# Optimization experiments

Hardware: AMD Instinct MI355X
Metric: run time of the kernel (lower is better)

## Reference

```python
import jax, jax.numpy as jnp
import numpy as np

NEG_SLOPE = 0.2


def gat_conv(x, edge_index, W, a_src, a_dst, b):
    # PyG GATConv (heads=1, add_self_loops=True, concat -> out_channels)
    N = x.shape[0]
    h = x @ W                                   # [N, F_out]
    loops = jnp.arange(N, dtype=edge_index.dtype)
    src = jnp.concatenate([edge_index[0], loops])   # message sources (x_j)
    dst = jnp.concatenate([edge_index[1], loops])   # message targets (x_i)
    # attention logits: e = LeakyReLU(a_src . h_j + a_dst . h_i)
    alpha_s = h @ a_src                          # [N]
    alpha_d = h @ a_dst                          # [N]
    e = jax.nn.leaky_relu(alpha_s[src] + alpha_d[dst], NEG_SLOPE)  # [E+N]
    # segment softmax over incoming edges of each dst node
    m = jax.ops.segment_max(e, dst, num_segments=N)
    e = jnp.exp(e - m[dst])
    denom = jax.ops.segment_sum(e, dst, num_segments=N)
    alpha = e / denom[dst]                       # self-loops guarantee denom > 0
    # weighted scatter-sum aggregation
    out = jax.ops.segment_sum(alpha[:, None] * h[src], dst, num_segments=N)
    return out + b


def setup_inputs() -> dict:
    key = jax.random.key(0)
    ks = jax.random.split(key, 10)
    N, E, F_in, H, F_out = 100000, 3200000, 54, 16, 16
    x = jax.random.normal(ks[0], (N, F_in), dtype=jnp.float32)
    edge_index = jax.random.randint(ks[1], (2, E), 0, N, dtype=jnp.int64)
    s1 = 1.0 / np.sqrt(F_in)
    s2 = 1.0 / np.sqrt(H)
    return {
        "x": x,
        "edge_index": edge_index,
        "W1": jax.random.uniform(ks[2], (F_in, H), jnp.float32, -s1, s1),
        "a1_src": jax.random.uniform(ks[3], (H,), jnp.float32, -s2, s2),
        "a1_dst": jax.random.uniform(ks[4], (H,), jnp.float32, -s2, s2),
        "b1": jnp.zeros((H,), jnp.float32),
        "W2": jax.random.uniform(ks[5], (H, F_out), jnp.float32, -s2, s2),
        "a2_src": jax.random.uniform(ks[6], (F_out,), jnp.float32, -0.25, 0.25),
        "a2_dst": jax.random.uniform(ks[7], (F_out,), jnp.float32, -0.25, 0.25),
        "b2": jnp.zeros((F_out,), jnp.float32),
    }


def reference(x, edge_index, W1, a1_src, a1_dst, b1, W2, a2_src, a2_dst, b2):
    h = gat_conv(x, edge_index, W1, a1_src, a1_dst, b1)
    h = jax.nn.elu(h)
    # dropout p=0.5 is identity in eval mode
    out = gat_conv(h, edge_index, W2, a2_src, a2_dst, b2)
    return out
```

## Files before the change

kernel.cpp:

```cpp
#include <hip/hip_runtime.h>
#include <hip/hip_bf16.h>

typedef __hip_bfloat16 bf16;

static constexpr int N_NODES = 100000;
static constexpr int N_EDGES = 3200000;
static constexpr int F_IN    = 54;
static constexpr int F_HID   = 16;

static constexpr int BSHIFT    = 7;
static constexpr int BNODES    = 128;
static constexpr int NBUCK     = (N_NODES + BNODES - 1) / BNODES;
static constexpr int CAP_B     = 5120;
static constexpr int BIN_CHUNK = 8192;
static constexpr int GRDB      = (N_EDGES + BIN_CHUNK - 1) / BIN_CHUNK;
static constexpr int GRDN_F    = (N_NODES + 1023) / 1024;

static constexpr size_t WS_FLAGS  = 0;
static constexpr size_t WS_ASRC   = 4;
static constexpr size_t WS_ADST   = 100004;
static constexpr size_t WS_ASRC2  = 200004;
static constexpr size_t WS_ADST2  = 300004;
static constexpr size_t WS_BCNT   = 400004;
static constexpr size_t WS_ROWBEG = 401028;
static constexpr size_t WS_ROWCNT = 501028;
static constexpr size_t WS_HBUF   = 601028;
static constexpr size_t WS_ZBUF   = 2201028;
static constexpr size_t WS_BEDGES = 3801028;
static constexpr size_t WS_SRCS   = 7804868;
static constexpr size_t WS_BUCKET_END = WS_SRCS + (size_t)NBUCK * CAP_B;
static constexpr size_t WS_ATOMIC_END = WS_ZBUF + 1600000;

__device__ __forceinline__ float lrelu(float v) { return v >= 0.f ? v : 0.2f * v; }
__device__ __forceinline__ float loadf(const void* p, int i, bool f32) {
    return f32 ? ((const float*)p)[i] : __bfloat162float(((const bf16*)p)[i]);
}

__global__ __launch_bounds__(256) void k_probe0(
    const void* __restrict__ x, const void* __restrict__ ei,
    int* __restrict__ flags, int* __restrict__ bcnt)
{
    __shared__ int cnt, nz;
    const int t = threadIdx.x;
    if (t == 0) { cnt = 0; nz = 0; }
    __syncthreads();
    const unsigned u = ((const unsigned*)x)[t];
    if ((u & 0x7FFFu) >= 0x4800u) atomicAdd(&cnt, 1);
    if (t < 64) {
        if (((const unsigned*)ei)[2 * t + 1] != 0u) atomicAdd(&nz, 1);
    }
    for (int i = t; i < 1024; i += 256) bcnt[i] = 0;
    __syncthreads();
    if (t == 0) flags[0] = ((cnt >= 16) ? 1 : 0) | ((nz == 0) ? 2 : 0);
}

__global__ __launch_bounds__(1024, 8) void k_binfeat(
    const void* __restrict__ ei, const void* __restrict__ x,
    const void* __restrict__ W1, const void* __restrict__ a_s,
    const void* __restrict__ a_d, const int* __restrict__ flags,
    int* __restrict__ bcnt, int* __restrict__ bedges,
    float* __restrict__ hbuf, float* __restrict__ asrc, float* __restrict__ adst)
{
    __shared__ int            hist[NBUCK];
    __shared__ int            base[NBUCK];
    __shared__ int            cval[BIN_CHUNK];
    __shared__ unsigned short cbkt[BIN_CHUNK];
    __shared__ float Wl[F_IN * F_HID];
    __shared__ float asl[F_HID];
    __shared__ float adl[F_HID];
    const int t = threadIdx.x;
    const bool f32 = flags[0] & 1;
    const bool i64 = flags[0] & 2;

    if (blockIdx.x < GRDB) {
        const int e0 = blockIdx.x * BIN_CHUNK;
        const int valid = min(BIN_CHUNK, N_EDGES - e0);
        for (int i = t; i < NBUCK; i += 1024) hist[i] = 0;
        __syncthreads();
#pragma unroll
        for (int i = 0; i < BIN_CHUNK / 1024; ++i) {
            const int idx = i * 1024 + t;
            const int e = e0 + idx;
            if (idx < valid) {
                int s, d;
                if (i64) {
                    s = ((const int*)ei)[2 * (size_t)e];
                    d = ((const int*)ei)[2 * ((size_t)N_EDGES + e)];
                } else {
                    s = ((const int*)ei)[e];
                    d = ((const int*)ei)[(size_t)N_EDGES + e];
                }
                const int b = d >> BSHIFT;
                cval[idx] = (s << BSHIFT) | (d & (BNODES - 1));
                cbkt[idx] = (unsigned short)b;
                atomicAdd(&hist[b], 1);
            }
        }
        __syncthreads();
        for (int i = t; i < NBUCK; i += 1024) {
            const int c = hist[i];
            base[i] = c ? atomicAdd(&bcnt[i], c) : 0;
            hist[i] = 0;
        }
        __syncthreads();
#pragma unroll
        for (int i = 0; i < BIN_CHUNK / 1024; ++i) {
            const int idx = i * 1024 + t;
            if (idx < valid) {
                const int b = cbkt[idx];
                const int r = atomicAdd(&hist[b], 1);
                const int pos = base[b] + r;
                if (pos < CAP_B) bedges[(size_t)b * CAP_B + pos] = cval[idx];
            }
        }
    } else {
        for (int i = t; i < F_IN * F_HID; i += 1024) Wl[i] = loadf(W1, i, f32);
        if (t < F_HID) { asl[t] = loadf(a_s, t, f32); adl[t] = loadf(a_d, t, f32); }
        __syncthreads();
        const int node = (blockIdx.x - GRDB) * 1024 + t;
        if (node >= N_NODES) return;

        float h[F_HID];
#pragma unroll
        for (int k = 0; k < F_HID; ++k) h[k] = 0.f;
        if (f32) {
            const float2* xp = (const float2*)((const float*)x + (size_t)node * F_IN);
#pragma unroll
            for (int j = 0; j < F_IN / 2; ++j) {
                const float2 v = xp[j];
#pragma unroll
                for (int k = 0; k < F_HID; ++k) {
                    h[k] = fmaf(v.x, Wl[(2*j)   * F_HID + k], h[k]);
                    h[k] = fmaf(v.y, Wl[(2*j+1) * F_HID + k], h[k]);
                }
            }
        } else {
            const unsigned* xu = (const unsigned*)x + (size_t)node * (F_IN / 2);
#pragma unroll
            for (int j = 0; j < F_IN / 2; ++j) {
                const unsigned u = xu[j];
                const float v0 = __uint_as_float(u << 16);
                const float v1 = __uint_as_float(u & 0xFFFF0000u);
#pragma unroll
                for (int k = 0; k < F_HID; ++k) {
                    h[k] = fmaf(v0, Wl[(2*j)   * F_HID + k], h[k]);
                    h[k] = fmaf(v1, Wl[(2*j+1) * F_HID + k], h[k]);
                }
            }
        }
        float s = 0.f, d = 0.f;
#pragma unroll
        for (int k = 0; k < F_HID; ++k) { s = fmaf(h[k], asl[k], s); d = fmaf(h[k], adl[k], d); }
        asrc[node] = s; adst[node] = d;
        float4* hb = (float4*)(hbuf + (size_t)node * F_HID);
#pragma unroll
        for (int q = 0; q < 4; ++q)
            hb[q] = make_float4(h[4*q], h[4*q+1], h[4*q+2], h[4*q+3]);
    }
}

__global__ __launch_bounds__(512) void k_bsort(
    const int* __restrict__ bcnt, const int* __restrict__ bedges,
    int* __restrict__ rowbeg, int* __restrict__ rowcnt, int* __restrict__ srcs)
{
    __shared__ int hist[BNODES];
    __shared__ int scan[BNODES];
    __shared__ int cur[BNODES];
    const int t = threadIdx.x;
    const int b = blockIdx.x;
    const int n0 = b << BSHIFT;
    if (t < BNODES) hist[t] = 0;
    __syncthreads();
    const int cnt = min(bcnt[b], CAP_B);
    const int* be = bedges + (size_t)b * CAP_B;
    for (int e = t; e < cnt; e += 512)
        atomicAdd(&hist[be[e] & (BNODES - 1)], 1);
    __syncthreads();
    if (t < BNODES) scan[t] = (hist[t] + 3) & ~3;
    __syncthreads();
#pragma unroll
    for (int off = 1; off < BNODES; off <<= 1) {
        const int v = (t < BNODES && t >= off) ? scan[t - off] : 0;
        __syncthreads();
        if (t < BNODES) scan[t] += v;
        __syncthreads();
    }
    if (t < BNODES) {
        const int ex = scan[t] - ((hist[t] + 3) & ~3);
        cur[t] = ex;
        const int node = n0 + t;
        if (node < N_NODES) {
            rowbeg[node] = b * CAP_B + ex;
            rowcnt[node] = hist[t];
        }
    }
    __syncthreads();
    for (int e = t; e < cnt; e += 512) {
        const int p = be[e];
        const int dl = p & (BNODES - 1);
        const int r = atomicAdd(&cur[dl], 1);
        if (r < CAP_B) srcs[(size_t)b * CAP_B + r] = p >> BSHIFT;
    }
}

__global__ __launch_bounds__(256) void k_agg1(
    const int* __restrict__ rowbeg, const int* __restrict__ rowcnt,
    const int* __restrict__ srcs,
    const float* __restrict__ asrc, const float* __restrict__ adst,
    const float* __restrict__ h, const void* __restrict__ b1,
    const void* __restrict__ W2, const void* __restrict__ a_s2,
    const void* __restrict__ a_d2, const int* __restrict__ flags,
    float* __restrict__ h2buf, float* __restrict__ asrc2, float* __restrict__ adst2)
{
    __shared__ float Wl[F_HID * F_HID];
    __shared__ float asl[F_HID];
    __shared__ float adl[F_HID];
    __shared__ float bl[F_HID];
    const bool f32 = flags[0] & 1;
    const int t = threadIdx.x;
    if (t < F_HID * F_HID) Wl[t] = loadf(W2, t, f32);
    if (t < F_HID) {
        asl[t] = loadf(a_s2, t, f32);
        adl[t] = loadf(a_d2, t, f32);
        bl[t]  = loadf(b1, t, f32);
    }
    __syncthreads();

    const int k = t & 15;
    const int node = blockIdx.x * 16 + (t >> 4);
    const float adn = adst[node];
    const float w0 = __expf(lrelu(asrc[node] + adn));
    float denom = w0;
    float acc = w0 * h[(size_t)node * F_HID + k];
    const int n = rowcnt[node];
    const int* sp = srcs + rowbeg[node];
    int i = 0;
    for (; i + 8 <= n; i += 8) {
        const int4 sa = *(const int4*)(sp + i);
        const int4 sb = *(const int4*)(sp + i + 4);
        const float a0 = asrc[sa.x], a1 = asrc[sa.y], a2 = asrc[sa.z], a3 = asrc[sa.w];
        const float a4 = asrc[sb.x], a5 = asrc[sb.y], a6 = asrc[sb.z], a7 = asrc[sb.w];
        const float h0 = h[(size_t)sa.x * F_HID + k];
        const float h1 = h[(size_t)sa.y * F_HID + k];
        const float h2 = h[(size_t)sa.z * F_HID + k];
        const float h3 = h[(size_t)sa.w * F_HID + k];
        const float h4 = h[(size_t)sb.x * F_HID + k];
        const float h5 = h[(size_t)sb.y * F_HID + k];
        const float h6 = h[(size_t)sb.z * F_HID + k];
        const float h7 = h[(size_t)sb.w * F_HID + k];
        const float e0 = __expf(lrelu(a0 + adn));
        const float e1 = __expf(lrelu(a1 + adn));
        const float e2 = __expf(lrelu(a2 + adn));
        const float e3 = __expf(lrelu(a3 + adn));
        const float e4 = __expf(lrelu(a4 + adn));
        const float e5 = __expf(lrelu(a5 + adn));
        const float e6 = __expf(lrelu(a6 + adn));
        const float e7 = __expf(lrelu(a7 + adn));
        denom += (e0 + e1 + e2 + e3) + (e4 + e5 + e6 + e7);
        acc = fmaf(e0, h0, acc); acc = fmaf(e1, h1, acc);
        acc = fmaf(e2, h2, acc); acc = fmaf(e3, h3, acc);
        acc = fmaf(e4, h4, acc); acc = fmaf(e5, h5, acc);
        acc = fmaf(e6, h6, acc); acc = fmaf(e7, h7, acc);
    }
    for (; i + 4 <= n; i += 4) {
        const int4 sa = *(const int4*)(sp + i);
        const float a0 = asrc[sa.x], a1 = asrc[sa.y], a2 = asrc[sa.z], a3 = asrc[sa.w];
        const float h0 = h[(size_t)sa.x * F_HID + k];
        const float h1 = h[(size_t)sa.y * F_HID + k];
        const float h2 = h[(size_t)sa.z * F_HID + k];
        const float h3 = h[(size_t)sa.w * F_HID + k];
        const float e0 = __expf(lrelu(a0 + adn));
        const float e1 = __expf(lrelu(a1 + adn));
        const float e2 = __expf(lrelu(a2 + adn));
        const float e3 = __expf(lrelu(a3 + adn));
        denom += (e0 + e1) + (e2 + e3);
        acc = fmaf(e0, h0, acc); acc = fmaf(e1, h1, acc);
        acc = fmaf(e2, h2, acc); acc = fmaf(e3, h3, acc);
    }
    for (; i < n; ++i) {
        const int s = sp[i];
        const float w = __expf(lrelu(asrc[s] + adn));
        denom += w;
        acc = fmaf(w, h[(size_t)s * F_HID + k], acc);
    }
    float z = acc / denom + bl[k];
    z = z > 0.f ? z : expm1f(z);

    float hh = 0.f;
#pragma unroll
    for (int j = 0; j < F_HID; ++j) {
        const float zj = __shfl(z, j, 16);
        hh = fmaf(zj, Wl[j * F_HID + k], hh);
    }
    float s2 = hh * asl[k], d2 = hh * adl[k];
#pragma unroll
    for (int off = 1; off < 16; off <<= 1) {
        s2 += __shfl_xor(s2, off, 16);
        d2 += __shfl_xor(d2, off, 16);
    }
    h2buf[(size_t)node * F_HID + k] = hh;
    if (k == 0) { asrc2[node] = s2; adst2[node] = d2; }
}

__global__ __launch_bounds__(256) void k_agg2(
    const int* __restrict__ rowbeg, const int* __restrict__ rowcnt,
    const int* __restrict__ srcs,
    const float* __restrict__ asrc, const float* __restrict__ adst,
    const float* __restrict__ h, const void* __restrict__ b2,
    const int* __restrict__ flags, float* __restrict__ outp)
{
    const bool f32 = flags[0] & 1;
    const int t = threadIdx.x;
    const int k = t & 15;
    const int node = blockIdx.x * 16 + (t >> 4);
    const float adn = adst[node];
    const float w0 = __expf(lrelu(asrc[node] + adn));
    float denom = w0;
    float acc = w0 * h[(size_t)node * F_HID + k];
    const int n = rowcnt[node];
    const int* sp = srcs + rowbeg[node];
    int i = 0;
    for (; i + 8 <= n; i += 8) {
        const int4 sa = *(const int4*)(sp + i);
        const int4 sb = *(const int4*)(sp + i + 4);
        const float a0 = asrc[sa.x], a1 = asrc[sa.y], a2 = asrc[sa.z], a3 = asrc[sa.w];
        const float a4 = asrc[sb.x], a5 = asrc[sb.y], a6 = asrc[sb.z], a7 = asrc[sb.w];
        const float h0 = h[(size_t)sa.x * F_HID + k];
        const float h1 = h[(size_t)sa.y * F_HID + k];
        const float h2 = h[(size_t)sa.z * F_HID + k];
        const float h3 = h[(size_t)sa.w * F_HID + k];
        const float h4 = h[(size_t)sb.x * F_HID + k];
        const float h5 = h[(size_t)sb.y * F_HID + k];
        const float h6 = h[(size_t)sb.z * F_HID + k];
        const float h7 = h[(size_t)sb.w * F_HID + k];
        const float e0 = __expf(lrelu(a0 + adn));
        const float e1 = __expf(lrelu(a1 + adn));
        const float e2 = __expf(lrelu(a2 + adn));
        const float e3 = __expf(lrelu(a3 + adn));
        const float e4 = __expf(lrelu(a4 + adn));
        const float e5 = __expf(lrelu(a5 + adn));
        const float e6 = __expf(lrelu(a6 + adn));
        const float e7 = __expf(lrelu(a7 + adn));
        denom += (e0 + e1 + e2 + e3) + (e4 + e5 + e6 + e7);
        acc = fmaf(e0, h0, acc); acc = fmaf(e1, h1, acc);
        acc = fmaf(e2, h2, acc); acc = fmaf(e3, h3, acc);
        acc = fmaf(e4, h4, acc); acc = fmaf(e5, h5, acc);
        acc = fmaf(e6, h6, acc); acc = fmaf(e7, h7, acc);
    }
    for (; i + 4 <= n; i += 4) {
        const int4 sa = *(const int4*)(sp + i);
        const float a0 = asrc[sa.x], a1 = asrc[sa.y], a2 = asrc[sa.z], a3 = asrc[sa.w];
        const float h0 = h[(size_t)sa.x * F_HID + k];
        const float h1 = h[(size_t)sa.y * F_HID + k];
        const float h2 = h[(size_t)sa.z * F_HID + k];
        const float h3 = h[(size_t)sa.w * F_HID + k];
        const float e0 = __expf(lrelu(a0 + adn));
        const float e1 = __expf(lrelu(a1 + adn));
        const float e2 = __expf(lrelu(a2 + adn));
        const float e3 = __expf(lrelu(a3 + adn));
        denom += (e0 + e1) + (e2 + e3);
        acc = fmaf(e0, h0, acc); acc = fmaf(e1, h1, acc);
        acc = fmaf(e2, h2, acc); acc = fmaf(e3, h3, acc);
    }
    for (; i < n; ++i) {
        const int s = sp[i];
        const float w = __expf(lrelu(asrc[s] + adn));
        denom += w;
        acc = fmaf(w, h[(size_t)s * F_HID + k], acc);
    }
    outp[(size_t)node * F_HID + k] = acc / denom + loadf(b2, k, f32);
}

__global__ __launch_bounds__(256) void k_feat1(
    const void* __restrict__ x, const void* __restrict__ W1,
    const void* __restrict__ a_s, const void* __restrict__ a_d,
    const int* __restrict__ flags,
    float* __restrict__ hbuf, float* __restrict__ asrc, float* __restrict__ adst)
{
    const bool f32 = flags[0] & 1;
    __shared__ float Wl[F_IN * F_HID];
    __shared__ float asl[F_HID];
    __shared__ float adl[F_HID];
    const int t = threadIdx.x;
    for (int i = t; i < F_IN * F_HID; i += 256) Wl[i] = loadf(W1, i, f32);
    if (t < F_HID) { asl[t] = loadf(a_s, t, f32); adl[t] = loadf(a_d, t, f32); }
    __syncthreads();
    const int node = blockIdx.x * 256 + t;
    if (node >= N_NODES) return;
    float h[F_HID];
#pragma unroll
    for (int k = 0; k < F_HID; ++k) h[k] = 0.f;
    if (f32) {
        const float2* xp = (const float2*)((const float*)x + (size_t)node * F_IN);
#pragma unroll
        for (int j = 0; j < F_IN / 2; ++j) {
            const float2 v = xp[j];
#pragma unroll
            for (int k = 0; k < F_HID; ++k) {
                h[k] = fmaf(v.x, Wl[(2*j)   * F_HID + k], h[k]);
                h[k] = fmaf(v.y, Wl[(2*j+1) * F_HID + k], h[k]);
            }
        }
    } else {
        const unsigned* xu = (const unsigned*)x + (size_t)node * (F_IN / 2);
#pragma unroll
        for (int j = 0; j < F_IN / 2; ++j) {
            const unsigned u = xu[j];
            const float v0 = __uint_as_float(u << 16);
            const float v1 = __uint_as_float(u & 0xFFFF0000u);
#pragma unroll
            for (int k = 0; k < F_HID; ++k) {
                h[k] = fmaf(v0, Wl[(2*j)   * F_HID + k], h[k]);
                h[k] = fmaf(v1, Wl[(2*j+1) * F_HID + k], h[k]);
            }
        }
    }
    float s = 0.f, d = 0.f;
#pragma unroll
    for (int k = 0; k < F_HID; ++k) { s = fmaf(h[k], asl[k], s); d = fmaf(h[k], adl[k], d); }
    asrc[node] = s; adst[node] = d;
    float4* hb = (float4*)(hbuf + (size_t)node * F_HID);
#pragma unroll
    for (int q = 0; q < 4; ++q)
        hb[q] = make_float4(h[4*q], h[4*q+1], h[4*q+2], h[4*q+3]);
}

__global__ __launch_bounds__(256) void k_selfinit(
    const float* __restrict__ asrc, const float* __restrict__ adst,
    const float* __restrict__ h, float* __restrict__ denom, float* __restrict__ acc)
{
    const int t = blockIdx.x * 256 + threadIdx.x;
    if (t >= N_NODES * F_HID) return;
    const int n = t >> 4;
    const float w0 = __expf(lrelu(asrc[n] + adst[n]));
    if ((t & 15) == 0) denom[n] = w0;
    acc[t] = w0 * h[t];
}

__global__ __launch_bounds__(256) void k_edge(
    const void* __restrict__ ei, const int* __restrict__ flags,
    const float* __restrict__ asrc, const float* __restrict__ adst,
    const float* __restrict__ hbuf,
    float* __restrict__ denom, float* __restrict__ acc)
{
    const int e = blockIdx.x * 256 + threadIdx.x;
    if (e >= N_EDGES) return;
    int s, d;
    if (flags[0] & 2) {
        const long long* e64 = (const long long*)ei;
        s = (int)e64[e]; d = (int)e64[(size_t)N_EDGES + e];
    } else {
        const int* e32 = (const int*)ei;
        s = e32[e]; d = e32[(size_t)N_EDGES + e];
    }
    const float w = __expf(lrelu(asrc[s] + adst[d]));
    atomicAdd(&denom[d], w);
    const float4* hs = (const float4*)(hbuf + (size_t)s * F_HID);
    float* ad = acc + (size_t)d * F_HID;
#pragma unroll
    for (int q = 0; q < 4; ++q) {
        const float4 hv = hs[q];
        atomicAdd(ad + 4*q + 0, w * hv.x);
        atomicAdd(ad + 4*q + 1, w * hv.y);
        atomicAdd(ad + 4*q + 2, w * hv.z);
        atomicAdd(ad + 4*q + 3, w * hv.w);
    }
}

__global__ __launch_bounds__(256) void k_div_elu(
    float* __restrict__ acc, const float* __restrict__ denom,
    const void* __restrict__ b1, const int* __restrict__ flags)
{
    const bool f32 = flags[0] & 1;
    const int t = blockIdx.x * 256 + threadIdx.x;
    if (t >= N_NODES * F_HID) return;
    const float v = acc[t] / denom[t >> 4] + loadf(b1, t & 15, f32);
    acc[t] = v > 0.f ? v : expm1f(v);
}

__global__ __launch_bounds__(256) void k_mid(
    const float* __restrict__ z,
    const void* __restrict__ W2, const void* __restrict__ a_s2,
    const void* __restrict__ a_d2, const int* __restrict__ flags,
    float* __restrict__ h2, float* __restrict__ asrc, float* __restrict__ adst)
{
    const bool f32 = flags[0] & 1;
    __shared__ float Wl[F_HID * F_HID];
    __shared__ float asl[F_HID];
    __shared__ float adl[F_HID];
    const int t = threadIdx.x;
    if (t < F_HID * F_HID) Wl[t] = loadf(W2, t, f32);
    if (t < F_HID) { asl[t] = loadf(a_s2, t, f32); adl[t] = loadf(a_d2, t, f32); }
    __syncthreads();
    const int node = blockIdx.x * 256 + t;
    if (node >= N_NODES) return;
    float zr[F_HID];
    const float4* zi = (const float4*)(z + (size_t)node * F_HID);
#pragma unroll
    for (int q = 0; q < 4; ++q) {
        const float4 zv = zi[q];
        zr[4*q+0]=zv.x; zr[4*q+1]=zv.y; zr[4*q+2]=zv.z; zr[4*q+3]=zv.w;
    }
    float h[F_HID];
#pragma unroll
    for (int k = 0; k < F_HID; ++k) h[k] = 0.f;
#pragma unroll
    for (int j = 0; j < F_HID; ++j) {
        const float zv = zr[j];
#pragma unroll
        for (int k = 0; k < F_HID; ++k) h[k] = fmaf(zv, Wl[j * F_HID + k], h[k]);
    }
    float s = 0.f, d = 0.f;
#pragma unroll
    for (int k = 0; k < F_HID; ++k) { s = fmaf(h[k], asl[k], s); d = fmaf(h[k], adl[k], d); }
    asrc[node] = s; adst[node] = d;
    float4* hb = (float4*)(h2 + (size_t)node * F_HID);
#pragma unroll
    for (int q = 0; q < 4; ++q)
        hb[q] = make_float4(h[4*q], h[4*q+1], h[4*q+2], h[4*q+3]);
}

__global__ __launch_bounds__(256) void k_out(
    const float* __restrict__ acc, const float* __restrict__ denom,
    const void* __restrict__ b2, const int* __restrict__ flags,
    float* __restrict__ out)
{
    const bool f32 = flags[0] & 1;
    const int t = blockIdx.x * 256 + threadIdx.x;
    if (t >= N_NODES * F_HID) return;
    out[t] = acc[t] / denom[t >> 4] + loadf(b2, t & 15, f32);
}

__global__ __launch_bounds__(256) void k_diag(float* __restrict__ out, float v)
{
    const int t = blockIdx.x * 256 + threadIdx.x;
    if (t < N_NODES * F_HID) out[t] = v;
}

extern "C" void kernel_launch(void* const* d_in, const int* in_sizes, int n_in,
                              void* d_out, int out_size, void* d_ws, size_t ws_size,
                              hipStream_t stream) {
    const void* x   = d_in[0];
    const void* ei  = d_in[1];
    const void* W1  = d_in[2];
    const void* a1s = d_in[3];
    const void* a1d = d_in[4];
    const void* b1  = d_in[5];
    const void* W2  = d_in[6];
    const void* a2s = d_in[7];
    const void* a2d = d_in[8];
    const void* b2  = d_in[9];
    float* out = (float*)d_out;

    float* ws     = (float*)d_ws;
    int*   flags  = (int*)(ws + WS_FLAGS);
    float* asrc   = ws + WS_ASRC;
    float* adst   = ws + WS_ADST;
    float* asrc2  = ws + WS_ASRC2;
    float* adst2  = ws + WS_ADST2;
    int*   bcnt   = (int*)(ws + WS_BCNT);
    int*   rowbeg = (int*)(ws + WS_ROWBEG);
    int*   rowcnt = (int*)(ws + WS_ROWCNT);
    float* hbuf   = ws + WS_HBUF;
    float* h2buf  = ws + WS_ZBUF;
    int*   bedges = (int*)(ws + WS_BEDGES);
    int*   srcs   = (int*)(ws + WS_SRCS);

    const dim3 blk(256);
    const dim3 grdN((N_NODES + 255) / 256);
    const dim3 grdE((N_EDGES + 255) / 256);
    const dim3 grdO((N_NODES * F_HID + 255) / 256);
    const dim3 grdBF(GRDB + GRDN_F);
    const dim3 grdS(NBUCK);
    const dim3 grdA(N_NODES / 16);

    if (ws_size >= WS_BUCKET_END * 4) {
        k_probe0 <<<dim3(1), blk, 0, stream>>>(x, ei, flags, bcnt);
        k_binfeat<<<grdBF, dim3(1024), 0, stream>>>(ei, x, W1, a1s, a1d, flags,
                                                    bcnt, bedges, hbuf, asrc, adst);
        k_bsort  <<<grdS, dim3(512), 0, stream>>>(bcnt, bedges, rowbeg, rowcnt, srcs);
        k_agg1   <<<grdA, blk, 0, stream>>>(rowbeg, rowcnt, srcs, asrc, adst, hbuf,
                                            b1, W2, a2s, a2d, flags,
                                            h2buf, asrc2, adst2);
        k_agg2   <<<grdA, blk, 0, stream>>>(rowbeg, rowcnt, srcs, asrc2, adst2,
                                            h2buf, b2, flags, out);
    } else if (ws_size >= WS_ATOMIC_END * 4) {
        float* acc   = h2buf;
        float* denom = asrc2;
        k_probe0 <<<dim3(1), blk, 0, stream>>>(x, ei, flags, bcnt);
        k_feat1  <<<grdN, blk, 0, stream>>>(x, W1, a1s, a1d, flags, hbuf, asrc, adst);
        k_selfinit<<<grdO, blk, 0, stream>>>(asrc, adst, hbuf, denom, acc);
        k_edge   <<<grdE, blk, 0, stream>>>(ei, flags, asrc, adst, hbuf, denom, acc);
        k_div_elu<<<grdO, blk, 0, stream>>>(acc, denom, b1, flags);
        k_mid    <<<grdN, blk, 0, stream>>>(acc, W2, a2s, a2d, flags, hbuf, asrc, adst);
        k_selfinit<<<grdO, blk, 0, stream>>>(asrc, adst, hbuf, denom, acc);
        k_edge   <<<grdE, blk, 0, stream>>>(ei, flags, asrc, adst, hbuf, denom, acc);
        k_out    <<<grdO, blk, 0, stream>>>(acc, denom, b2, flags, out);
    } else {
        k_diag<<<grdO, blk, 0, stream>>>(out, (float)(ws_size >> 10));
    }
}
```

Measured before the change: 274.4 us.

## Store features as bf16 and precompute exponentials to remove per-edge exp

Node features are now stored in bf16, which halves the bytes fetched by the edge gathers in both aggregation kernels. Per-source exp(s) and exp(0.2*s) are precomputed, so each edge weight becomes a compare plus a multiply instead of an exp. This works because exp(lrelu(s+d)) factors into per-node terms. The 4-wide tail loop is dropped. The cost is lower precision in the hidden features, a possible overflow risk from exponentiating logits without max-subtraction, and a larger float2 gather for the source term.

```diff
diff --git a/kernel.cpp b/kernel.cpp
--- a/kernel.cpp
+++ b/kernel.cpp
@@ -17,23 +17,31 @@
 static constexpr int GRDN_F    = (N_NODES + 1023) / 1024;
 
 static constexpr size_t WS_FLAGS  = 0;
-static constexpr size_t WS_ASRC   = 4;
-static constexpr size_t WS_ADST   = 100004;
-static constexpr size_t WS_ASRC2  = 200004;
-static constexpr size_t WS_ADST2  = 300004;
-static constexpr size_t WS_BCNT   = 400004;
-static constexpr size_t WS_ROWBEG = 401028;
-static constexpr size_t WS_ROWCNT = 501028;
-static constexpr size_t WS_HBUF   = 601028;
-static constexpr size_t WS_ZBUF   = 2201028;
-static constexpr size_t WS_BEDGES = 3801028;
-static constexpr size_t WS_SRCS   = 7804868;
+static constexpr size_t WS_EASRC  = 4;
+static constexpr size_t WS_ADST   = 200004;
+static constexpr size_t WS_EASRC2 = 300004;
+static constexpr size_t WS_ADST2  = 500004;
+static constexpr size_t WS_BCNT   = 600004;
+static constexpr size_t WS_ROWBEG = 601028;
+static constexpr size_t WS_ROWCNT = 701028;
+static constexpr size_t WS_HBUF   = 801028;
+static constexpr size_t WS_H2BUF  = 1601028;
+static constexpr size_t WS_BEDGES = 2401028;
+static constexpr size_t WS_SRCS   = 6404868;
 static constexpr size_t WS_BUCKET_END = WS_SRCS + (size_t)NBUCK * CAP_B;
-static constexpr size_t WS_ATOMIC_END = WS_ZBUF + 1600000;
+static constexpr size_t WS_FB_DEN     = 4001028;
+static constexpr size_t WS_ATOMIC_END = 4101028;
 
 __device__ __forceinline__ float lrelu(float v) { return v >= 0.f ? v : 0.2f * v; }
 __device__ __forceinline__ float loadf(const void* p, int i, bool f32) {
     return f32 ? ((const float*)p)[i] : __bfloat162float(((const bf16*)p)[i]);
+}
+__device__ __forceinline__ unsigned short f2bf(float f) {
+    unsigned u = __float_as_uint(f);
+    return (unsigned short)((u + 0x7FFFu + ((u >> 16) & 1u)) >> 16);
+}
+__device__ __forceinline__ float bf2f(unsigned short b) {
+    return __uint_as_float((unsigned)b << 16);
 }
 
 __global__ __launch_bounds__(256) void k_probe0(
@@ -59,7 +67,8 @@
     const void* __restrict__ W1, const void* __restrict__ a_s,
     const void* __restrict__ a_d, const int* __restrict__ flags,
     int* __restrict__ bcnt, int* __restrict__ bedges,
-    float* __restrict__ hbuf, float* __restrict__ asrc, float* __restrict__ adst)
+    unsigned short* __restrict__ hbuf, float2* __restrict__ easrc,
+    float* __restrict__ adst)
 {
     __shared__ int            hist[NBUCK];
     __shared__ int            base[NBUCK];
@@ -151,11 +160,15 @@
         float s = 0.f, d = 0.f;
 #pragma unroll
         for (int k = 0; k < F_HID; ++k) { s = fmaf(h[k], asl[k], s); d = fmaf(h[k], adl[k], d); }
-        asrc[node] = s; adst[node] = d;
-        float4* hb = (float4*)(hbuf + (size_t)node * F_HID);
-#pragma unroll
-        for (int q = 0; q < 4; ++q)
-            hb[q] = make_float4(h[4*q], h[4*q+1], h[4*q+2], h[4*q+3]);
+        easrc[node] = make_float2(__expf(s), __expf(0.2f * s));
+        adst[node] = d;
+        unsigned pk[8];
+#pragma unroll
+        for (int q = 0; q < 8; ++q)
+            pk[q] = (unsigned)f2bf(h[2*q]) | ((unsigned)f2bf(h[2*q+1]) << 16);
+        uint4* hb = (uint4*)(hbuf + (size_t)node * F_HID);
+        hb[0] = make_uint4(pk[0], pk[1], pk[2], pk[3]);
+        hb[1] = make_uint4(pk[4], pk[5], pk[6], pk[7]);
     }
 }
 
@@ -206,11 +219,12 @@
 __global__ __launch_bounds__(256) void k_agg1(
     const int* __restrict__ rowbeg, const int* __restrict__ rowcnt,
     const int* __restrict__ srcs,
-    const float* __restrict__ asrc, const float* __restrict__ adst,
-    const float* __restrict__ h, const void* __restrict__ b1,
+    const float2* __restrict__ easrc, const float* __restrict__ adst,
+    const unsigned short* __restrict__ h, const void* __restrict__ b1,
     const void* __restrict__ W2, const void* __restrict__ a_s2,
     const void* __restrict__ a_d2, const int* __restrict__ flags,
-    float* __restrict__ h2buf, float* __restrict__ asrc2, float* __restrict__ adst2)
+    unsigned short* __restrict__ h2buf, float2* __restrict__ easrc2,
+    float* __restrict__ adst2)
 {
     __shared__ float Wl[F_HID * F_HID];
     __shared__ float asl[F_HID];
@@ -228,60 +242,52 @@
 
     const int k = t & 15;
     const int node = blockIdx.x * 16 + (t >> 4);
-    const float adn = adst[node];
-    const float w0 = __expf(lrelu(asrc[node] + adn));
+    const float adn  = adst[node];
+    const float Ead  = __expf(adn);
+    const float F5ad = __expf(0.2f * adn);
+    const float T    = __expf(-adn);
+    const float2 es  = easrc[node];
+    const float w0 = (es.x >= T) ? es.x * Ead : es.y * F5ad;
     float denom = w0;
-    float acc = w0 * h[(size_t)node * F_HID + k];
+    float acc = w0 * bf2f(h[(size_t)node * F_HID + k]);
     const int n = rowcnt[node];
     const int* sp = srcs + rowbeg[node];
     int i = 0;
     for (; i + 8 <= n; i += 8) {
         const int4 sa = *(const int4*)(sp + i);
         const int4 sb = *(const int4*)(sp + i + 4);
-        const float a0 = asrc[sa.x], a1 = asrc[sa.y], a2 = asrc[sa.z], a3 = asrc[sa.w];
-        const float a4 = asrc[sb.x], a5 = asrc[sb.y], a6 = asrc[sb.z], a7 = asrc[sb.w];
-        const float h0 = h[(size_t)sa.x * F_HID + k];
-        const float h1 = h[(size_t)sa.y * F_HID + k];
-        const float h2 = h[(size_t)sa.z * F_HID + k];
-        const float h3 = h[(size_t)sa.w * F_HID + k];
-        const float h4 = h[(size_t)sb.x * F_HID + k];
-        const float h5 = h[(size_t)sb.y * F_HID + k];
-        const float h6 = h[(size_t)sb.z * F_HID + k];
-        const float h7 = h[(size_t)sb.w * F_HID + k];
-        const float e0 = __expf(lrelu(a0 + adn));
-        const float e1 = __expf(lrelu(a1 + adn));
-        const float e2 = __expf(lrelu(a2 + adn));
-        const float e3 = __expf(lrelu(a3 + adn));
-        const float e4 = __expf(lrelu(a4 + adn));
-        const float e5 = __expf(lrelu(a5 + adn));
-        const float e6 = __expf(lrelu(a6 + adn));
-        const float e7 = __expf(lrelu(a7 + adn));
+        const float2 ea0 = easrc[sa.x], ea1 = easrc[sa.y];
+        const float2 ea2 = easrc[sa.z], ea3 = easrc[sa.w];
+        const float2 ea4 = easrc[sb.x], ea5 = easrc[sb.y];
+        const float2 ea6 = easrc[sb.z], ea7 = easrc[sb.w];
+        const float h0 = bf2f(h[(size_t)sa.x * F_HID + k]);
+        const float h1 = bf2f(h[(size_t)sa.y * F_HID + k]);
+        const float h2 = bf2f(h[(size_t)sa.z * F_HID + k]);
+        const float h3 = bf2f(h[(size_t)sa.w * F_HID + k]);
+        const float h4 = bf2f(h[(size_t)sb.x * F_HID + k]);
+        const float h5 = bf2f(h[(size_t)sb.y * F_HID + k]);
+        const float h6 = bf2f(h[(size_t)sb.z * F_HID + k]);
+        const float h7 = bf2f(h[(size_t)sb.w * F_HID + k]);
+        const float e0 = (ea0.x >= T) ? ea0.x * Ead : ea0.y * F5ad;
+        const float e1 = (ea1.x >= T) ? ea1.x * Ead : ea1.y * F5ad;
+        const float e2 = (ea2.x >= T) ? ea2.x * Ead : ea2.y * F5ad;
+        const float e3 = (ea3.x >= T) ? ea3.x * Ead : ea3.y * F5ad;
+        const float e4 = (ea4.x >= T) ? ea4.x * Ead : ea4.y * F5ad;
+        const float e5 = (ea5.x >= T) ? ea5.x * Ead : ea5.y * F5ad;
+        const float e6 = (ea6.x >= T) ? ea6.x * Ead : ea6.y * F5ad;
+        const float e7 = (ea7.x >= T) ? ea7.x * Ead : ea7.y * F5ad;
         denom += (e0 + e1 + e2 + e3) + (e4 + e5 + e6 + e7);
         acc = fmaf(e0, h0, acc); acc = fmaf(e1, h1, acc);
         acc = fmaf(e2, h2, acc); acc = fmaf(e3, h3, acc);
         acc = fmaf(e4, h4, acc); acc = fmaf(e5, h5, acc);
         acc = fmaf(e6, h6, acc); acc = fmaf(e7, h7, acc);
     }
-    for (; i + 4 <= n; i += 4) {
-        const int4 sa = *(const int4*)(sp + i);
-        const float a0 = asrc[sa.x], a1 = asrc[sa.y], a2 = asrc[sa.z], a3 = asrc[sa.w];
-        const float h0 = h[(size_t)sa.x * F_HID + k];
-        const float h1 = h[(size_t)sa.y * F_HID + k];
-        const float h2 = h[(size_t)sa.z * F_HID + k];
-        const float h3 = h[(size_t)sa.w * F_HID + k];
-        const float e0 = __expf(lrelu(a0 + adn));
-        const float e1 = __expf(lrelu(a1 + adn));
-        const float e2 = __expf(lrelu(a2 + adn));
-        const float e3 = __expf(lrelu(a3 + adn));
-        denom += (e0 + e1) + (e2 + e3);
-        acc = fmaf(e0, h0, acc); acc = fmaf(e1, h1, acc);
-        acc = fmaf(e2, h2, acc); acc = fmaf(e3, h3, acc);
-    }
     for (; i < n; ++i) {
         const int s = sp[i];
-        const float w = __expf(lrelu(asrc[s] + adn));
+        const float2 ea = easrc[s];
+        const float w = (ea.x >= T) ? ea.x * Ead : ea.y * F5ad;
         denom += w;
-        acc = fmaf(w, h[(size_t)s * F_HID + k], acc);
+        acc = fmaf(w, bf2f(h[(size_t)s * F_HID + k]), acc);
     }
     float z = acc / denom + bl[k];
     z = z > 0.f ? z : expm1f(z);
@@ -298,75 +304,70 @@
         s2 += __shfl_xor(s2, off, 16);
         d2 += __shfl_xor(d2, off, 16);
     }
-    h2buf[(size_t)node * F_HID + k] = hh;
-    if (k == 0) { asrc2[node] = s2; adst2[node] = d2; }
+    h2buf[(size_t)node * F_HID + k] = f2bf(hh);
+    if (k == 0) {
+        easrc2[node] = make_float2(__expf(s2), __expf(0.2f * s2));
+        adst2[node] = d2;
+    }
 }
 
 __global__ __launch_bounds__(256) void k_agg2(
     const int* __restrict__ rowbeg, const int* __restrict__ rowcnt,
     const int* __restrict__ srcs,
-    const float* __restrict__ asrc, const float* __restrict__ adst,
-    const float* __restrict__ h, const void* __restrict__ b2,
+    const float2* __restrict__ easrc, const float* __restrict__ adst,
+    const unsigned short* __restrict__ h, const void* __restrict__ b2,
     const int* __restrict__ flags, float* __restrict__ outp)
 {
     const bool f32 = flags[0] & 1;
     const int t = threadIdx.x;
     const int k = t & 15;
     const int node = blockIdx.x * 16 + (t >> 4);
-    const float adn = adst[node];
-    const float w0 = __expf(lrelu(asrc[node] + adn));
+    const float adn  = adst[node];
+    const float Ead  = __expf(adn);
+    const float F5ad = __expf(0.2f * adn);
+    const float T    = __expf(-adn);
+    const float2 es  = easrc[node];
+    const float w0 = (es.x >= T) ? es.x * Ead : es.y * F5ad;
     float denom = w0;
-    float acc = w0 * h[(size_t)node * F_HID + k];
+    float acc = w0 * bf2f(h[(size_t)node * F_HID + k]);
     const int n = rowcnt[node];
     const int* sp = srcs + rowbeg[node];
     int i = 0;
     for (; i + 8 <= n; i += 8) {
         const int4 sa = *(const int4*)(sp + i);
         const int4 sb = *(const int4*)(sp + i + 4);
-        const float a0 = asrc[sa.x], a1 = asrc[sa.y], a2 = asrc[sa.z], a3 = asrc[sa.w];
-        const float a4 = asrc[sb.x], a5 = asrc[sb.y], a6 = asrc[sb.z], a7 = asrc[sb.w];
-        const float h0 = h[(size_t)sa.x * F_HID + k];
-        const float h1 = h[(size_t)sa.y * F_HID + k];
-        const float h2 = h[(size_t)sa.z * F_HID + k];
-        const float h3 = h[(size_t)sa.w * F_HID + k];
-        const float h4 = h[(size_t)sb.x * F_HID + k];
-        const float h5 = h[(size_t)sb.y * F_HID + k];
-        const float h6 = h[(size_t)sb.z * F_HID + k];
-        const float h7 = h[(size_t)sb.w * F_HID + k];
-        const float e0 = __expf(lrelu(a0 + adn));
-        const float e1 = __expf(lrelu(a1 + adn));
-        const float e2 = __expf(lrelu(a2 + adn));
-        const float e3 = __expf(lrelu(a3 + adn));
-        const float e4 = __expf(lrelu(a4 + adn));
-        const float e5 = __expf(lrelu(a5 + adn));
-        const float e6 = __expf(lrelu(a6 + adn));
-        const float e7 = __expf(lrelu(a7 + adn));
+        const float2 ea0 = easrc[sa.x], ea1 = easrc[sa.y];
+        const float2 ea2 = easrc[sa.z], ea3 = easrc[sa.w];
+        const float2 ea4 = easrc[sb.x], ea5 = easrc[sb.y];
+        const float2 ea6 = easrc[sb.z], ea7 = easrc[sb.w];
+        const float h0 = bf2f(h[(size_t)sa.x * F_HID + k]);
+        const float h1 = bf2f(h[(size_t)sa.y * F_HID + k]);
+        const float h2 = bf2f(h[(size_t)sa.z * F_HID + k]);
+        const float h3 = bf2f(h[(size_t)sa.w * F_HID + k]);
+        const float h4 = bf2f(h[(size_t)sb.x * F_HID + k]);
+        const float h5 = bf2f(h[(size_t)sb.y * F_HID + k]);
+        const float h6 = bf2f(h[(size_t)sb.z * F_HID + k]);
+        const float h7 = bf2f(h[(size_t)sb.w * F_HID + k]);
+        const float e0 = (ea0.x >= T) ? ea0.x * Ead : ea0.y * F5ad;
+        const float e1 = (ea1.x >= T) ? ea1.x * Ead : ea1.y * F5ad;
+        const float e2 = (ea2.x >= T) ? ea2.x * Ead : ea2.y * F5ad;
+        const float e3 = (ea3.x >= T) ? ea3.x * Ead : ea3.y * F5ad;
+        const float e4 = (ea4.x >= T) ? ea4.x * Ead : ea4.y * F5ad;
+        const float e5 = (ea5.x >= T) ? ea5.x * Ead : ea5.y * F5ad;
+        const float e6 = (ea6.x >= T) ? ea6.x * Ead : ea6.y * F5ad;
+        const float e7 = (ea7.x >= T) ? ea7.x * Ead : ea7.y * F5ad;
         denom += (e0 + e1 + e2 + e3) + (e4 + e5 + e6 + e7);
         acc = fmaf(e0, h0, acc); acc = fmaf(e1, h1, acc);
         acc = fmaf(e2, h2, acc); acc = fmaf(e3, h3, acc);
         acc = fmaf(e4, h4, acc); acc = fmaf(e5, h5, acc);
         acc = fmaf(e6, h6, acc); acc = fmaf(e7, h7, acc);
     }
-    for (; i + 4 <= n; i += 4) {
-        const int4 sa = *(const int4*)(sp + i);
-        const float a0 = asrc[sa.x], a1 = asrc[sa.y], a2 = asrc[sa.z], a3 = asrc[sa.w];
-        const float h0 = h[(size_t)sa.x * F_HID + k];
-        const float h1 = h[(size_t)sa.y * F_HID + k];
-        const float h2 = h[(size_t)sa.z * F_HID + k];
-        const float h3 = h[(size_t)sa.w * F_HID + k];
-        const float e0 = __expf(lrelu(a0 + adn));
-        const float e1 = __expf(lrelu(a1 + adn));
-        const float e2 = __expf(lrelu(a2 + adn));
-        const float e3 = __expf(lrelu(a3 + adn));
-        denom += (e0 + e1) + (e2 + e3);
-        acc = fmaf(e0, h0, acc); acc = fmaf(e1, h1, acc);
-        acc = fmaf(e2, h2, acc); acc = fmaf(e3, h3, acc);
-    }
     for (; i < n; ++i) {
         const int s = sp[i];
-        const float w = __expf(lrelu(asrc[s] + adn));
+        const float2 ea = easrc[s];
+        const float w = (ea.x >= T) ? ea.x * Ead : ea.y * F5ad;
         denom += w;
-        acc = fmaf(w, h[(size_t)s * F_HID + k], acc);
+        acc = fmaf(w, bf2f(h[(size_t)s * F_HID + k]), acc);
     }
     outp[(size_t)node * F_HID + k] = acc / denom + loadf(b2, k, f32);
 }
@@ -552,19 +553,19 @@
     const void* b2  = d_in[9];
     float* out = (float*)d_out;
 
-    float* ws     = (float*)d_ws;
-    int*   flags  = (int*)(ws + WS_FLAGS);
-    float* asrc   = ws + WS_ASRC;
-    float* adst   = ws + WS_ADST;
-    float* asrc2  = ws + WS_ASRC2;
-    float* adst2  = ws + WS_ADST2;
-    int*   bcnt   = (int*)(ws + WS_BCNT);
-    int*   rowbeg = (int*)(ws + WS_ROWBEG);
-    int*   rowcnt = (int*)(ws + WS_ROWCNT);
-    float* hbuf   = ws + WS_HBUF;
-    float* h2buf  = ws + WS_ZBUF;
-    int*   bedges = (int*)(ws + WS_BEDGES);
-    int*   srcs   = (int*)(ws + WS_SRCS);
+    float* ws = (float*)d_ws;
+    int*    flags  = (int*)(ws + WS_FLAGS);
+    float2* easrc  = (float2*)(ws + WS_EASRC);
+    float*  adst   = ws + WS_ADST;
+    float2* easrc2 = (float2*)(ws + WS_EASRC2);
+    float*  adst2  = ws + WS_ADST2;
+    int*    bcnt   = (int*)(ws + WS_BCNT);
+    int*    rowbeg = (int*)(ws + WS_ROWBEG);
+    int*    rowcnt = (int*)(ws + WS_ROWCNT);
+    unsigned short* hbuf  = (unsigned short*)(ws + WS_HBUF);
+    unsigned short* h2buf = (unsigned short*)(ws + WS_H2BUF);
+    int*    bedges = (int*)(ws + WS_BEDGES);
+    int*    srcs   = (int*)(ws + WS_SRCS);
 
     const dim3 blk(256);
     const dim3 grdN((N_NODES + 255) / 256);
@@ -577,25 +578,28 @@
     if (ws_size >= WS_BUCKET_END * 4) {
         k_probe0 <<<dim3(1), blk, 0, stream>>>(x, ei, flags, bcnt);
         k_binfeat<<<grdBF, dim3(1024), 0, stream>>>(ei, x, W1, a1s, a1d, flags,
-                                                    bcnt, bedges, hbuf, asrc, adst);
+                                                    bcnt, bedges, hbuf, easrc, adst);
         k_bsort  <<<grdS, dim3(512), 0, stream>>>(bcnt, bedges, rowbeg, rowcnt, srcs);
-        k_agg1   <<<grdA, blk, 0, stream>>>(rowbeg, rowcnt, srcs, asrc, adst, hbuf,
+        k_agg1   <<<grdA, blk, 0, stream>>>(rowbeg, rowcnt, srcs, easrc, adst, hbuf,
                                             b1, W2, a2s, a2d, flags,
-                                            h2buf, asrc2, adst2);
-        k_agg2   <<<grdA, blk, 0, stream>>>(rowbeg, rowcnt, srcs, asrc2, adst2,
+                                            h2buf, easrc2, adst2);
+        k_agg2   <<<grdA, blk, 0, stream>>>(rowbeg, rowcnt, srcs, easrc2, adst2,
                                             h2buf, b2, flags, out);
     } else if (ws_size >= WS_ATOMIC_END * 4) {
-        float* acc   = h2buf;
-        float* denom = asrc2;
+        float* fb_h   = ws + WS_HBUF;
+        float* fb_acc = ws + WS_BEDGES;
+        float* fb_den = ws + WS_FB_DEN;
+        float* fb_as  = ws + WS_EASRC;
+        float* fb_ad  = ws + WS_ADST;
         k_probe0 <<<dim3(1), blk, 0, stream>>>(x, ei, flags, bcnt);
-        k_feat1  <<<grdN, blk, 0, stream>>>(x, W1, a1s, a1d, flags, hbuf, asrc, adst);
-        k_selfinit<<<grdO, blk, 0, stream>>>(asrc, adst, hbuf, denom, acc);
-        k_edge   <<<grdE, blk, 0, stream>>>(ei, flags, asrc, adst, hbuf, denom, acc);
-        k_div_elu<<<grdO, blk, 0, stream>>>(acc, denom, b1, flags);
-        k_mid    <<<grdN, blk, 0, stream>>>(acc, W2, a2s, a2d, flags, hbuf, asrc, adst);
-        k_selfinit<<<grdO, blk, 0, stream>>>(asrc, adst, hbuf, denom, acc);
-        k_edge   <<<grdE, blk, 0, stream>>>(ei, flags, asrc, adst, hbuf, denom, acc);
-        k_out    <<<grdO, blk, 0, stream>>>(acc, denom, b2, flags, out);
+        k_feat1  <<<grdN, blk, 0, stream>>>(x, W1, a1s, a1d, flags, fb_h, fb_as, fb_ad);
+        k_selfinit<<<grdO, blk, 0, stream>>>(fb_as, fb_ad, fb_h, fb_den, fb_acc);
+        k_edge   <<<grdE, blk, 0, stream>>>(ei, flags, fb_as, fb_ad, fb_h, fb_den, fb_acc);
+        k_div_elu<<<grdO, blk, 0, stream>>>(fb_acc, fb_den, b1, flags);
+        k_mid    <<<grdN, blk, 0, stream>>>(fb_acc, W2, a2s, a2d, flags, fb_h, fb_as, fb_ad);
+        k_selfinit<<<grdO, blk, 0, stream>>>(fb_as, fb_ad, fb_h, fb_den, fb_acc);
+        k_edge   <<<grdE, blk, 0, stream>>>(ei, flags, fb_as, fb_ad, fb_h, fb_den, fb_acc);
+        k_out    <<<grdO, blk, 0, stream>>>(fb_acc, fb_den, b2, flags, out);
     } else {
         k_diag<<<grdO, blk, 0, stream>>>(out, (float)(ws_size >> 10));
     }
```

Measured after the change: 296.6 us. +8.1%, slower.
